# Kernel optimization log

Measured on AMD Instinct MI355X. Metric: run time of the kernel, lower is better.

The kernel has to match this reference:

```python
import jax, jax.numpy as jnp
import numpy as np

B, N, D, OUT = 4, 512, 128, 128

def setup_inputs() -> dict:
    key = jax.random.key(0)
    k1, k2, k3, k4 = jax.random.split(key, 4)
    x = jax.random.normal(k1, (B, N, D), dtype=jnp.float32)
    # binary adjacency mask (float, as it multiplies edge features in the original)
    adj = (jax.random.uniform(k2, (B, N, N)) < 0.5).astype(jnp.float32)
    # nn.Linear(2D, OUT): store as (2D, OUT) so y = feat @ W + b
    W = jax.random.normal(k3, (2 * D, OUT), dtype=jnp.float32) * (1.0 / np.sqrt(2 * D))
    b = jax.random.normal(k4, (OUT,), dtype=jnp.float32) * 0.01
    return {"x": x, "adj": adj, "W": W, "b": b}

def reference(x, adj, W, b):
    # edge_feat = cat([x_i, x_j - x_i]); linear on concat decomposes as
    # x_i @ W1 + (x_j - x_i) @ W2 = x_i @ (W1 - W2) + x_j @ W2  -> avoids the (B,N,N,2D) concat.
    d = x.shape[-1]
    W1, W2 = W[:d], W[d:]
    p = jnp.einsum('bnd,do->bno', x, W1 - W2)   # contribution of x_i
    q = jnp.einsum('bnd,do->bno', x, W2)        # contribution of x_j
    pre = p[:, :, None, :] + q[:, None, :, :] + b  # (B, N, N, OUT)
    h = jax.nn.relu(pre) * adj[..., None]          # dropout is identity in eval mode
    return jnp.max(h, axis=2)                      # max over neighbors j -> (B, N, OUT)
```

## Files before the change

kernel.cpp:

```cpp
#include <hip/hip_runtime.h>

#define B_ 4
#define N_ 512
#define D_ 128
#define O_ 128

#define R1 8

__global__ __launch_bounds__(1024)
void gemm_pq_kernel(const float* __restrict__ x, const float* __restrict__ W,
                    const float* __restrict__ bias, float* __restrict__ q,
                    float* __restrict__ phat) {
    const int tid = threadIdx.x;
    const int o2  = (tid & 63) * 2;
    const int kq  = __builtin_amdgcn_readfirstlane(tid >> 6);
    const int row0 = blockIdx.x * R1;
    const int k0   = kq * 8;

    const float* __restrict__ xb = x + (size_t)row0 * D_;

    float2 w1v[8], w2v[8];
#pragma unroll
    for (int kk = 0; kk < 8; ++kk) {
        w1v[kk] = *(const float2*)&W[(size_t)(k0 + kk) * O_ + o2];
        w2v[kk] = *(const float2*)&W[(size_t)(k0 + kk + D_) * O_ + o2];
    }
    float2 wd[8];
#pragma unroll
    for (int kk = 0; kk < 8; ++kk) {
        wd[kk].x = w1v[kk].x - w2v[kk].x;
        wd[kk].y = w1v[kk].y - w2v[kk].y;
    }

    float accp[R1][2], accq[R1][2];
#pragma unroll
    for (int r = 0; r < R1; ++r) {
        accp[r][0] = 0.0f; accp[r][1] = 0.0f;
        accq[r][0] = 0.0f; accq[r][1] = 0.0f;
    }

#pragma unroll
    for (int r = 0; r < R1; ++r) {
#pragma unroll
        for (int kk = 0; kk < 8; ++kk) {
            const float xv = xb[(size_t)r * D_ + k0 + kk];
            accp[r][0] = fmaf(xv, wd[kk].x,  accp[r][0]);
            accp[r][1] = fmaf(xv, wd[kk].y,  accp[r][1]);
            accq[r][0] = fmaf(xv, w2v[kk].x, accq[r][0]);
            accq[r][1] = fmaf(xv, w2v[kk].y, accq[r][1]);
        }
    }

    __shared__ float redq[R1][16][O_ + 2];
    __shared__ float redp[R1][16][O_ + 2];

#pragma unroll
    for (int r = 0; r < R1; ++r) {
        *(float2*)&redq[r][kq][o2] = make_float2(accq[r][0], accq[r][1]);
        *(float2*)&redp[r][kq][o2] = make_float2(accp[r][0], accp[r][1]);
    }
    __syncthreads();

    {
        const int rr = tid >> 7;
        const int oo = tid & (O_ - 1);
        float sq = 0.0f, sp = 0.0f;
#pragma unroll
        for (int p = 0; p < 16; ++p) { sq += redq[rr][p][oo]; sp += redp[rr][p][oo]; }
        const size_t idx = (size_t)(row0 + rr) * O_ + oo;
        q[idx]    = sq;
        phat[idx] = sp + bias[oo];
    }
}

#define TI 8

__global__ __launch_bounds__(1024)
void maskmax_kernel(const float* __restrict__ q, const float* __restrict__ phat,
                    const float* __restrict__ adj, float* __restrict__ out) {
    const int tid = threadIdx.x;
    const int o2  = (tid & 63) * 2;
    const int jq  = __builtin_amdgcn_readfirstlane(tid >> 6);
    const int b   = blockIdx.x >> 6;
    const int i0  = (blockIdx.x & 63) * TI;
    const int j0  = jq * 32;

    const float* __restrict__ qb   = q + (size_t)b * N_ * O_ + o2;
    const float* __restrict__ arow = adj + ((size_t)b * N_ + i0) * N_ + j0;

    float2 qv[32];
#pragma unroll
    for (int u = 0; u < 32; ++u)
        qv[u] = *(const float2*)&qb[(size_t)(j0 + u) * O_];

    float m[TI][2];
#pragma unroll
    for (int i = 0; i < TI; ++i) { m[i][0] = -1e30f; m[i][1] = -1e30f; }

#pragma unroll
    for (int i = 0; i < TI; ++i) {
        const float* __restrict__ ar = arow + (size_t)i * N_;
        float mx = m[i][0], my = m[i][1];
#pragma unroll
        for (int u = 0; u < 32; u += 2) {
            const float a0 = ar[u], a1 = ar[u + 1];
            const float c0x = fmaf(a0, 1024.0f, qv[u].x);
            const float c0y = fmaf(a0, 1024.0f, qv[u].y);
            const float c1x = fmaf(a1, 1024.0f, qv[u + 1].x);
            const float c1y = fmaf(a1, 1024.0f, qv[u + 1].y);
            mx = fmaxf(mx, fmaxf(c0x, c1x));
            my = fmaxf(my, fmaxf(c0y, c1y));
        }
        m[i][0] = mx; m[i][1] = my;
    }

    __shared__ float part[TI][16][O_ + 2];
#pragma unroll
    for (int i = 0; i < TI; ++i)
        *(float2*)&part[i][jq][o2] = make_float2(m[i][0], m[i][1]);
    __syncthreads();

    {
        const int i  = tid >> 7;
        const int oo = tid & (O_ - 1);
        float mm = -1e30f;
#pragma unroll
        for (int p = 0; p < 16; ++p) mm = fmaxf(mm, part[i][p][oo]);
        const size_t idx = ((size_t)b * N_ + i0 + i) * O_ + oo;
        const float v = phat[idx] + mm - 1024.0f;
        out[idx] = v > 0.0f ? v : 0.0f;
    }
}

extern "C" void kernel_launch(void* const* d_in, const int* in_sizes, int n_in,
                              void* d_out, int out_size, void* d_ws, size_t ws_size,
                              hipStream_t stream) {
    const float* x    = (const float*)d_in[0];
    const float* adj  = (const float*)d_in[1];
    const float* W    = (const float*)d_in[2];
    const float* bias = (const float*)d_in[3];
    float* out = (float*)d_out;

    float* q    = (float*)d_ws;
    float* phat = q + (size_t)B_ * N_ * O_;

    gemm_pq_kernel<<<(B_ * N_) / R1, 1024, 0, stream>>>(x, W, bias, q, phat);
    maskmax_kernel<<<B_ * (N_ / TI), 1024, 0, stream>>>(q, phat, adj, out);
}
```

Baseline: 77.60 us.

## Fuse GEMM and masked max into one kernel with output-slice tiling

Replaces the two-kernel pipeline (GEMM writing q/phat to workspace, then masked-max reading them) with a single fused kernel. Each block handles one batch, a 64-row i-tile and a 16-wide output slice, recomputes q for all 512 j in shared memory and p only for its own rows, then does the masked max against adj. This removes the workspace round trip and a launch, at the cost of recomputing the q GEMM for each of the 8 i-tiles (8x redundant GEMM work) and rereading adj once per output slice (8x adj traffic, mostly from L2).

```diff
diff --git a/kernel.cpp b/kernel.cpp
--- a/kernel.cpp
+++ b/kernel.cpp
@@ -4,131 +4,153 @@
 #define N_ 512
 #define D_ 128
 #define O_ 128
+#define OS 16
+#define IT 64
 
-#define R1 8
+__global__ __launch_bounds__(1024, 4)
+void edgeconv_fused(const float* __restrict__ x, const float* __restrict__ adj,
+                    const float* __restrict__ W, const float* __restrict__ bias,
+                    float* __restrict__ out) {
+    __shared__ float W2s[D_][OS];
+    __shared__ float Wds[D_][OS];
+    __shared__ float qsT[OS][N_ + 4];
+    __shared__ float phs[IT][OS];
+    __shared__ float part[IT][OS][5];
 
-__global__ __launch_bounds__(1024)
-void gemm_pq_kernel(const float* __restrict__ x, const float* __restrict__ W,
-                    const float* __restrict__ bias, float* __restrict__ q,
-                    float* __restrict__ phat) {
-    const int tid = threadIdx.x;
-    const int o2  = (tid & 63) * 2;
-    const int kq  = __builtin_amdgcn_readfirstlane(tid >> 6);
-    const int row0 = blockIdx.x * R1;
-    const int k0   = kq * 8;
+    const int tid   = threadIdx.x;
+    const int bid   = blockIdx.x;
+    const int os    = bid & 7;
+    const int it    = (bid >> 3) & 7;
+    const int b     = bid >> 6;
+    const int obase = os * OS;
+    const int i0    = it * IT;
 
-    const float* __restrict__ xb = x + (size_t)row0 * D_;
+    {
+        const int k  = tid >> 3;
+        const int oc = (tid & 7) * 2;
+        const float2 w1 = *(const float2*)&W[(size_t)k * O_ + obase + oc];
+        const float2 w2 = *(const float2*)&W[(size_t)(k + D_) * O_ + obase + oc];
+        *(float2*)&W2s[k][oc] = w2;
+        *(float2*)&Wds[k][oc] = make_float2(w1.x - w2.x, w1.y - w2.y);
+    }
+    __syncthreads();
 
-    float2 w1v[8], w2v[8];
+    const int jb  = (tid >> 2) * 2;
+    const int oq4 = (tid & 3) * 4;
+    const float* __restrict__ X0 = x + ((size_t)b * N_ + jb) * D_;
+    const float* __restrict__ X1 = X0 + D_;
+
+    float aq[2][4] = {{0,0,0,0},{0,0,0,0}};
+    float ap[2][4] = {{0,0,0,0},{0,0,0,0}};
+    const bool in_tile = (jb >= i0) && (jb < i0 + IT);
+
+    if (in_tile) {
+#pragma unroll 4
+        for (int kc = 0; kc < 16; ++kc) {
+            float xr0[8], xr1[8];
+            *(float4*)&xr0[0] = *(const float4*)&X0[kc * 8];
+            *(float4*)&xr0[4] = *(const float4*)&X0[kc * 8 + 4];
+            *(float4*)&xr1[0] = *(const float4*)&X1[kc * 8];
+            *(float4*)&xr1[4] = *(const float4*)&X1[kc * 8 + 4];
 #pragma unroll
-    for (int kk = 0; kk < 8; ++kk) {
-        w1v[kk] = *(const float2*)&W[(size_t)(k0 + kk) * O_ + o2];
-        w2v[kk] = *(const float2*)&W[(size_t)(k0 + kk + D_) * O_ + o2];
-    }
-    float2 wd[8];
+            for (int kk = 0; kk < 8; ++kk) {
+                const float4 wq = *(const float4*)&W2s[kc * 8 + kk][oq4];
+                const float4 wd = *(const float4*)&Wds[kc * 8 + kk][oq4];
+                const float x0 = xr0[kk], x1 = xr1[kk];
+                aq[0][0] = fmaf(x0, wq.x, aq[0][0]);
+                aq[0][1] = fmaf(x0, wq.y, aq[0][1]);
+                aq[0][2] = fmaf(x0, wq.z, aq[0][2]);
+                aq[0][3] = fmaf(x0, wq.w, aq[0][3]);
+                aq[1][0] = fmaf(x1, wq.x, aq[1][0]);
+                aq[1][1] = fmaf(x1, wq.y, aq[1][1]);
+                aq[1][2] = fmaf(x1, wq.z, aq[1][2]);
+                aq[1][3] = fmaf(x1, wq.w, aq[1][3]);
+                ap[0][0] = fmaf(x0, wd.x, ap[0][0]);
+                ap[0][1] = fmaf(x0, wd.y, ap[0][1]);
+                ap[0][2] = fmaf(x0, wd.z, ap[0][2]);
+                ap[0][3] = fmaf(x0, wd.w, ap[0][3]);
+                ap[1][0] = fmaf(x1, wd.x, ap[1][0]);
+                ap[1][1] = fmaf(x1, wd.y, ap[1][1]);
+                ap[1][2] = fmaf(x1, wd.z, ap[1][2]);
+                ap[1][3] = fmaf(x1, wd.w, ap[1][3]);
+            }
+        }
+    } else {
+#pragma unroll 4
+        for (int kc = 0; kc < 16; ++kc) {
+            float xr0[8], xr1[8];
+            *(float4*)&xr0[0] = *(const float4*)&X0[kc * 8];
+            *(float4*)&xr0[4] = *(const float4*)&X0[kc * 8 + 4];
+            *(float4*)&xr1[0] = *(const float4*)&X1[kc * 8];
+            *(float4*)&xr1[4] = *(const float4*)&X1[kc * 8 + 4];
 #pragma unroll
-    for (int kk = 0; kk < 8; ++kk) {
-        wd[kk].x = w1v[kk].x - w2v[kk].x;
-        wd[kk].y = w1v[kk].y - w2v[kk].y;
-    }
-
-    float accp[R1][2], accq[R1][2];
-#pragma unroll
-    for (int r = 0; r < R1; ++r) {
-        accp[r][0] = 0.0f; accp[r][1] = 0.0f;
-        accq[r][0] = 0.0f; accq[r][1] = 0.0f;
+            for (int kk = 0; kk < 8; ++kk) {
+                const float4 wq = *(const float4*)&W2s[kc * 8 + kk][oq4];
+                const float x0 = xr0[kk], x1 = xr1[kk];
+                aq[0][0] = fmaf(x0, wq.x, aq[0][0]);
+                aq[0][1] = fmaf(x0, wq.y, aq[0][1]);
+                aq[0][2] = fmaf(x0, wq.z, aq[0][2]);
+                aq[0][3] = fmaf(x0, wq.w, aq[0][3]);
+                aq[1][0] = fmaf(x1, wq.x, aq[1][0]);
+                aq[1][1] = fmaf(x1, wq.y, aq[1][1]);
+                aq[1][2] = fmaf(x1, wq.z, aq[1][2]);
+                aq[1][3] = fmaf(x1, wq.w, aq[1][3]);
+            }
+        }
     }
 
 #pragma unroll
-    for (int r = 0; r < R1; ++r) {
+    for (int c = 0; c < 4; ++c)
+        *(float2*)&qsT[oq4 + c][jb] = make_float2(aq[0][c], aq[1][c]);
+
+    if (in_tile) {
+        const int il = jb - i0;
 #pragma unroll
-        for (int kk = 0; kk < 8; ++kk) {
-            const float xv = xb[(size_t)r * D_ + k0 + kk];
-            accp[r][0] = fmaf(xv, wd[kk].x,  accp[r][0]);
-            accp[r][1] = fmaf(xv, wd[kk].y,  accp[r][1]);
-            accq[r][0] = fmaf(xv, w2v[kk].x, accq[r][0]);
-            accq[r][1] = fmaf(xv, w2v[kk].y, accq[r][1]);
+        for (int c = 0; c < 4; ++c) {
+            phs[il][oq4 + c]     = ap[0][c];
+            phs[il + 1][oq4 + c] = ap[1][c];
         }
-    }
-
-    __shared__ float redq[R1][16][O_ + 2];
-    __shared__ float redp[R1][16][O_ + 2];
-
-#pragma unroll
-    for (int r = 0; r < R1; ++r) {
-        *(float2*)&redq[r][kq][o2] = make_float2(accq[r][0], accq[r][1]);
-        *(float2*)&redp[r][kq][o2] = make_float2(accp[r][0], accp[r][1]);
     }
     __syncthreads();
 
     {
-        const int rr = tid >> 7;
-        const int oo = tid & (O_ - 1);
-        float sq = 0.0f, sp = 0.0f;
-#pragma unroll
-        for (int p = 0; p < 16; ++p) { sq += redq[rr][p][oo]; sp += redp[rr][p][oo]; }
-        const size_t idx = (size_t)(row0 + rr) * O_ + oo;
-        q[idx]    = sq;
-        phat[idx] = sp + bias[oo];
+        const int oo = tid & 15;
+        const int js = (tid >> 4) & 3;
+        const int ib = (tid >> 6) * 4;
+        const float* __restrict__ arow = adj + ((size_t)b * N_ + i0 + ib) * N_;
+
+        float m0 = -1e30f, m1 = -1e30f, m2 = -1e30f, m3 = -1e30f;
+#pragma unroll 2
+        for (int t = 0; t < 32; ++t) {
+            const int j4 = js * 4 + t * 16;
+            const float4 qv = *(const float4*)&qsT[oo][j4];
+            const float4 a0 = *(const float4*)&arow[0 * N_ + j4];
+            const float4 a1 = *(const float4*)&arow[1 * N_ + j4];
+            const float4 a2 = *(const float4*)&arow[2 * N_ + j4];
+            const float4 a3 = *(const float4*)&arow[3 * N_ + j4];
+            m0 = fmaxf(m0, fmaxf(fmaxf(fmaf(a0.x, 1024.0f, qv.x), fmaf(a0.y, 1024.0f, qv.y)),
+                                 fmaxf(fmaf(a0.z, 1024.0f, qv.z), fmaf(a0.w, 1024.0f, qv.w))));
+            m1 = fmaxf(m1, fmaxf(fmaxf(fmaf(a1.x, 1024.0f, qv.x), fmaf(a1.y, 1024.0f, qv.y)),
+                                 fmaxf(fmaf(a1.z, 1024.0f, qv.z), fmaf(a1.w, 1024.0f, qv.w))));
+            m2 = fmaxf(m2, fmaxf(fmaxf(fmaf(a2.x, 1024.0f, qv.x), fmaf(a2.y, 1024.0f, qv.y)),
+                                 fmaxf(fmaf(a2.z, 1024.0f, qv.z), fmaf(a2.w, 1024.0f, qv.w))));
+            m3 = fmaxf(m3, fmaxf(fmaxf(fmaf(a3.x, 1024.0f, qv.x), fmaf(a3.y, 1024.0f, qv.y)),
+                                 fmaxf(fmaf(a3.z, 1024.0f, qv.z), fmaf(a3.w, 1024.0f, qv.w))));
+        }
+        part[ib + 0][oo][js] = m0;
+        part[ib + 1][oo][js] = m1;
+        part[ib + 2][oo][js] = m2;
+        part[ib + 3][oo][js] = m3;
     }
-}
-
-#define TI 8
-
-__global__ __launch_bounds__(1024)
-void maskmax_kernel(const float* __restrict__ q, const float* __restrict__ phat,
-                    const float* __restrict__ adj, float* __restrict__ out) {
-    const int tid = threadIdx.x;
-    const int o2  = (tid & 63) * 2;
-    const int jq  = __builtin_amdgcn_readfirstlane(tid >> 6);
-    const int b   = blockIdx.x >> 6;
-    const int i0  = (blockIdx.x & 63) * TI;
-    const int j0  = jq * 32;
-
-    const float* __restrict__ qb   = q + (size_t)b * N_ * O_ + o2;
-    const float* __restrict__ arow = adj + ((size_t)b * N_ + i0) * N_ + j0;
-
-    float2 qv[32];
-#pragma unroll
-    for (int u = 0; u < 32; ++u)
-        qv[u] = *(const float2*)&qb[(size_t)(j0 + u) * O_];
-
-    float m[TI][2];
-#pragma unroll
-    for (int i = 0; i < TI; ++i) { m[i][0] = -1e30f; m[i][1] = -1e30f; }
-
-#pragma unroll
-    for (int i = 0; i < TI; ++i) {
-        const float* __restrict__ ar = arow + (size_t)i * N_;
-        float mx = m[i][0], my = m[i][1];
-#pragma unroll
-        for (int u = 0; u < 32; u += 2) {
-            const float a0 = ar[u], a1 = ar[u + 1];
-            const float c0x = fmaf(a0, 1024.0f, qv[u].x);
-            const float c0y = fmaf(a0, 1024.0f, qv[u].y);
-            const float c1x = fmaf(a1, 1024.0f, qv[u + 1].x);
-            const float c1y = fmaf(a1, 1024.0f, qv[u + 1].y);
-            mx = fmaxf(mx, fmaxf(c0x, c1x));
-            my = fmaxf(my, fmaxf(c0y, c1y));
-        }
-        m[i][0] = mx; m[i][1] = my;
-    }
-
-    __shared__ float part[TI][16][O_ + 2];
-#pragma unroll
-    for (int i = 0; i < TI; ++i)
-        *(float2*)&part[i][jq][o2] = make_float2(m[i][0], m[i][1]);
     __syncthreads();
 
     {
-        const int i  = tid >> 7;
-        const int oo = tid & (O_ - 1);
-        float mm = -1e30f;
-#pragma unroll
-        for (int p = 0; p < 16; ++p) mm = fmaxf(mm, part[i][p][oo]);
-        const size_t idx = ((size_t)b * N_ + i0 + i) * O_ + oo;
-        const float v = phat[idx] + mm - 1024.0f;
-        out[idx] = v > 0.0f ? v : 0.0f;
+        const int il = tid >> 4;
+        const int oo = tid & 15;
+        const float mm = fmaxf(fmaxf(part[il][oo][0], part[il][oo][1]),
+                               fmaxf(part[il][oo][2], part[il][oo][3]));
+        const float v = phs[il][oo] + bias[obase + oo] + mm - 1024.0f;
+        out[((size_t)b * N_ + i0 + il) * O_ + obase + oo] = fmaxf(v, 0.0f);
     }
 }
 
@@ -141,9 +163,7 @@
     const float* bias = (const float*)d_in[3];
     float* out = (float*)d_out;
 
-    float* q    = (float*)d_ws;
-    float* phat = q + (size_t)B_ * N_ * O_;
+    (void)d_ws; (void)ws_size;
 
-    gemm_pq_kernel<<<(B_ * N_) / R1, 1024, 0, stream>>>(x, W, bias, q, phat);
-    maskmax_kernel<<<B_ * (N_ / TI), 1024, 0, stream>>>(q, phat, adj, out);
+    edgeconv_fused<<<B_ * 8 * 8, 1024, 0, stream>>>(x, adj, W, bias, out);
 }
```

Result: slower. 94.04 us (+21.2%).
